# Kernel optimization log

Measured on AMD Instinct MI355X. Metric: run time of the kernel, lower is better.

Reference implementation:

```python
import jax, jax.numpy as jnp
import numpy as np

N_SYM = 128
BATCH = 131072
LEVERAGE = 30.0


def setup_inputs() -> dict:
    key = jax.random.key(0)
    ks = jax.random.split(key, 8)
    fractions = jax.random.normal(ks[0], (N_SYM, BATCH), dtype=jnp.float32)
    # exec_samples are Bernoulli(0/1) execution indicators, kept as float
    exec_samples = jnp.round(jax.random.uniform(ks[1], (N_SYM, BATCH), dtype=jnp.float32))
    pos_sizes = jax.random.normal(ks[2], (N_SYM, BATCH), dtype=jnp.float32)
    # margin rates strictly positive
    margin_rates = jax.random.uniform(ks[3], (N_SYM, BATCH), dtype=jnp.float32) * 0.9 + 0.1
    unused_margin = jax.random.uniform(ks[4], (BATCH,), dtype=jnp.float32) * 1000.0
    # per-symbol volume constraints: min == step (typical broker config), max >> min
    msm_step = jax.random.uniform(ks[5], (N_SYM,), dtype=jnp.float32) * 0.01 + 0.01
    msm_min = msm_step
    msm_max = msm_step * 1000.0
    return {
        "fractions": fractions,
        "exec_samples": exec_samples,
        "pos_sizes": pos_sizes,
        "margin_rates": margin_rates,
        "unused_margin": unused_margin,
        "msm_min": msm_min,
        "msm_step": msm_step,
        "msm_max": msm_max,
    }


def reference(fractions, exec_samples, pos_sizes, margin_rates, unused_margin,
              msm_min, msm_step, msm_max):
    """JAX port of LowLevelInferenceEngine._compute_new_pos_sizes.

    Sequential recurrence over traded symbols (axis 0), carrying
    unused_margin [BATCH]. Returns (new_pos_sizes [N_SYM, BATCH],
    final unused_margin [BATCH]).
    """

    def step_fn(um, xs):
        frac, ex, pos, mr, mn, st, mx = xs
        unused_size = um * mr * LEVERAGE
        max_pos_size = jnp.abs(pos) + unused_size
        # torch.where(pos*frac > 0, unused_size, max_pos_size).minimum(0)
        adj = jnp.minimum(jnp.where(pos * frac > 0, unused_size, max_pos_size), 0.0)
        new_pos_size = frac * (max_pos_size - adj)
        abs_nps = jnp.abs(new_pos_size)
        sgn = jnp.sign(new_pos_size)
        abs_nps = jnp.floor(abs_nps / st) * st
        abs_nps = jnp.where(abs_nps < mn, 0.0, abs_nps)
        abs_nps = jnp.minimum(abs_nps, mx)
        out = ex * (sgn * abs_nps) + (1.0 - ex) * pos
        um_new = (max_pos_size - abs_nps) / (mr * LEVERAGE)
        return um_new, out

    um_final, new_pos_sizes = jax.lax.scan(
        step_fn,
        unused_margin,
        (fractions, exec_samples, pos_sizes, margin_rates, msm_min, msm_step, msm_max),
    )
    return new_pos_sizes, um_final
```

## Files before the change

kernel.cpp:

```cpp
#include <hip/hip_runtime.h>
#include <math.h>

#define N_SYM 128
#define BATCH 131072
#define B4    (BATCH / 4)
#define LEV   30.0f
#define D     4

typedef float v4 __attribute__((ext_vector_type(4)));

__device__ __forceinline__ float step1(float f, float e, float p, float m,
                                       float st, float mn, float mx,
                                       float* um)
{
    const float mrl = m * LEV;
    const float us  = *um * mrl;
    const float mps = fabsf(p) + us;
    const float adj = fminf((p * f > 0.0f) ? us : mps, 0.0f);
    const float nps = f * (mps - adj);

    float       a  = fabsf(nps);
    const float sg = copysignf(1.0f, nps);
    a = floorf(a / st) * st;
    a = (a < mn) ? 0.0f : a;
    a = fminf(a, mx);

    *um = (mps - a) / mrl;
    return e * (sg * a) + (1.0f - e) * p;
}

__global__ __launch_bounds__(64) void lle_scan_kernel(
    const float* __restrict__ frac,
    const float* __restrict__ exs,
    const float* __restrict__ pos,
    const float* __restrict__ mrate,
    const float* __restrict__ um0,
    const float* __restrict__ msm_min,
    const float* __restrict__ msm_step,
    const float* __restrict__ msm_max,
    float* __restrict__ out)
{
    const size_t c4 = (size_t)(blockIdx.x * 64 + threadIdx.x);

    const v4* F = (const v4*)frac;
    const v4* E = (const v4*)exs;
    const v4* P = (const v4*)pos;
    const v4* M = (const v4*)mrate;
    v4*       O = (v4*)out;

    const v4 umv = __builtin_nontemporal_load((const v4*)um0 + c4);
    float um[4] = {umv.x, umv.y, umv.z, umv.w};

    v4 fb[D], eb[D], pb[D], mb[D];

#pragma unroll
    for (int j = 0; j < D; ++j) {
        const size_t o = (size_t)j * B4 + c4;
        fb[j] = __builtin_nontemporal_load(F + o);
        eb[j] = __builtin_nontemporal_load(E + o);
        pb[j] = __builtin_nontemporal_load(P + o);
        mb[j] = __builtin_nontemporal_load(M + o);
    }

    for (int s0 = 0; s0 < N_SYM - D; s0 += D) {
#pragma unroll
        for (int j = 0; j < D; ++j) {
            const int s = s0 + j;
            const v4 f = fb[j];
            const v4 e = eb[j];
            const v4 p = pb[j];
            const v4 m = mb[j];

            {
                const size_t o = (size_t)(s + D) * B4 + c4;
                fb[j] = __builtin_nontemporal_load(F + o);
                eb[j] = __builtin_nontemporal_load(E + o);
                pb[j] = __builtin_nontemporal_load(P + o);
                mb[j] = __builtin_nontemporal_load(M + o);
            }

            const float st = msm_step[s];
            const float mn = msm_min[s];
            const float mx = msm_max[s];

            v4 r;
            r.x = step1(f.x, e.x, p.x, m.x, st, mn, mx, &um[0]);
            r.y = step1(f.y, e.y, p.y, m.y, st, mn, mx, &um[1]);
            r.z = step1(f.z, e.z, p.z, m.z, st, mn, mx, &um[2]);
            r.w = step1(f.w, e.w, p.w, m.w, st, mn, mx, &um[3]);

            __builtin_nontemporal_store(r, O + (size_t)s * B4 + c4);
        }
    }

#pragma unroll
    for (int j = 0; j < D; ++j) {
        const int s = N_SYM - D + j;
        const v4 f = fb[j];
        const v4 e = eb[j];
        const v4 p = pb[j];
        const v4 m = mb[j];

        const float st = msm_step[s];
        const float mn = msm_min[s];
        const float mx = msm_max[s];

        v4 r;
        r.x = step1(f.x, e.x, p.x, m.x, st, mn, mx, &um[0]);
        r.y = step1(f.y, e.y, p.y, m.y, st, mn, mx, &um[1]);
        r.z = step1(f.z, e.z, p.z, m.z, st, mn, mx, &um[2]);
        r.w = step1(f.w, e.w, p.w, m.w, st, mn, mx, &um[3]);

        __builtin_nontemporal_store(r, O + (size_t)s * B4 + c4);
    }

    v4 umo;
    umo.x = um[0]; umo.y = um[1]; umo.z = um[2]; umo.w = um[3];
    __builtin_nontemporal_store(umo, O + (size_t)N_SYM * B4 + c4);
}

extern "C" void kernel_launch(void* const* d_in, const int* in_sizes, int n_in,
                              void* d_out, int out_size, void* d_ws, size_t ws_size,
                              hipStream_t stream) {
    const float* frac     = (const float*)d_in[0];
    const float* exs      = (const float*)d_in[1];
    const float* pos      = (const float*)d_in[2];
    const float* mrate    = (const float*)d_in[3];
    const float* um0      = (const float*)d_in[4];
    const float* msm_min  = (const float*)d_in[5];
    const float* msm_step = (const float*)d_in[6];
    const float* msm_max  = (const float*)d_in[7];
    float* out = (float*)d_out;

    const int block = 64;
    const int grid  = (BATCH / 4) / block;

    hipLaunchKernelGGL(lle_scan_kernel, dim3(grid), dim3(block), 0, stream,
                       frac, exs, pos, mrate, um0, msm_min, msm_step, msm_max,
                       out);
}
```

Measured before the change: 259.2 us.

## Add helper prefetch wavefronts that warm cache ahead of compute wave

Each block now has one compute wavefront running the scan and four helper wavefronts, one per input stream. The helpers load rows a few symbols ahead of the compute wave's progress, which they track through a shared volatile counter, so the data is already in cache when the compute wave reads it. The compute wave's loads also change from nontemporal to normal so they can hit those cached lines. The aim is to hide memory latency on the serial recurrence, at the cost of extra load traffic, spin-wait sleeps and possible cache thrashing if helpers run too far ahead.

```diff
diff --git a/kernel.cpp b/kernel.cpp
--- a/kernel.cpp
+++ b/kernel.cpp
@@ -6,6 +6,7 @@
 #define B4    (BATCH / 4)
 #define LEV   30.0f
 #define D     4
+#define PD    8
 
 typedef float v4 __attribute__((ext_vector_type(4)));
 
@@ -29,7 +30,7 @@
     return e * (sg * a) + (1.0f - e) * p;
 }
 
-__global__ __launch_bounds__(64) void lle_scan_kernel(
+__global__ __launch_bounds__(320) void lle_pf_kernel(
     const float* __restrict__ frac,
     const float* __restrict__ exs,
     const float* __restrict__ pos,
@@ -40,7 +41,11 @@
     const float* __restrict__ msm_max,
     float* __restrict__ out)
 {
-    const size_t c4 = (size_t)(blockIdx.x * 64 + threadIdx.x);
+    __shared__ volatile int prog;
+
+    const int    wv   = threadIdx.x >> 6;
+    const int    lane = threadIdx.x & 63;
+    const size_t c4   = (size_t)blockIdx.x * 64 + lane;
 
     const v4* F = (const v4*)frac;
     const v4* E = (const v4*)exs;
@@ -48,36 +53,57 @@
     const v4* M = (const v4*)mrate;
     v4*       O = (v4*)out;
 
-    const v4 umv = __builtin_nontemporal_load((const v4*)um0 + c4);
-    float um[4] = {umv.x, umv.y, umv.z, umv.w};
+    if (wv == 0) {
+        if (lane == 0) prog = -1;
 
-    v4 fb[D], eb[D], pb[D], mb[D];
+        const v4 umv = *((const v4*)um0 + c4);
+        float um[4] = {umv.x, umv.y, umv.z, umv.w};
+
+        v4 fb[D], eb[D], pb[D], mb[D];
 
 #pragma unroll
-    for (int j = 0; j < D; ++j) {
-        const size_t o = (size_t)j * B4 + c4;
-        fb[j] = __builtin_nontemporal_load(F + o);
-        eb[j] = __builtin_nontemporal_load(E + o);
-        pb[j] = __builtin_nontemporal_load(P + o);
-        mb[j] = __builtin_nontemporal_load(M + o);
-    }
+        for (int j = 0; j < D; ++j) {
+            const size_t o = (size_t)j * B4 + c4;
+            fb[j] = F[o]; eb[j] = E[o]; pb[j] = P[o]; mb[j] = M[o];
+        }
 
-    for (int s0 = 0; s0 < N_SYM - D; s0 += D) {
+        for (int s0 = 0; s0 < N_SYM - D; s0 += D) {
+#pragma unroll
+            for (int j = 0; j < D; ++j) {
+                const int s = s0 + j;
+                if (lane == 0) prog = s;
+                const v4 f = fb[j];
+                const v4 e = eb[j];
+                const v4 p = pb[j];
+                const v4 m = mb[j];
+
+                {
+                    const size_t o = (size_t)(s + D) * B4 + c4;
+                    fb[j] = F[o]; eb[j] = E[o]; pb[j] = P[o]; mb[j] = M[o];
+                }
+
+                const float st = msm_step[s];
+                const float mn = msm_min[s];
+                const float mx = msm_max[s];
+
+                v4 r;
+                r.x = step1(f.x, e.x, p.x, m.x, st, mn, mx, &um[0]);
+                r.y = step1(f.y, e.y, p.y, m.y, st, mn, mx, &um[1]);
+                r.z = step1(f.z, e.z, p.z, m.z, st, mn, mx, &um[2]);
+                r.w = step1(f.w, e.w, p.w, m.w, st, mn, mx, &um[3]);
+
+                __builtin_nontemporal_store(r, O + (size_t)s * B4 + c4);
+            }
+        }
+
 #pragma unroll
         for (int j = 0; j < D; ++j) {
-            const int s = s0 + j;
+            const int s = N_SYM - D + j;
+            if (lane == 0) prog = s;
             const v4 f = fb[j];
             const v4 e = eb[j];
             const v4 p = pb[j];
             const v4 m = mb[j];
-
-            {
-                const size_t o = (size_t)(s + D) * B4 + c4;
-                fb[j] = __builtin_nontemporal_load(F + o);
-                eb[j] = __builtin_nontemporal_load(E + o);
-                pb[j] = __builtin_nontemporal_load(P + o);
-                mb[j] = __builtin_nontemporal_load(M + o);
-            }
 
             const float st = msm_step[s];
             const float mn = msm_min[s];
@@ -91,32 +117,26 @@
 
             __builtin_nontemporal_store(r, O + (size_t)s * B4 + c4);
         }
+
+        v4 umo;
+        umo.x = um[0]; umo.y = um[1]; umo.z = um[2]; umo.w = um[3];
+        __builtin_nontemporal_store(umo, O + (size_t)N_SYM * B4 + c4);
+    } else {
+        const v4* SRC = (wv == 1) ? F : (wv == 2) ? E : (wv == 3) ? P : M;
+
+        __builtin_amdgcn_s_sleep(32);
+
+        for (int g = 0; g < N_SYM / 4; ++g) {
+            const int s = g * 4;
+            while (s > prog + PD) __builtin_amdgcn_s_sleep(8);
+
+            const v4 a = SRC[(size_t)(s + 0) * B4 + c4];
+            const v4 b = SRC[(size_t)(s + 1) * B4 + c4];
+            const v4 c = SRC[(size_t)(s + 2) * B4 + c4];
+            const v4 d = SRC[(size_t)(s + 3) * B4 + c4];
+            asm volatile("" :: "v"(a), "v"(b), "v"(c), "v"(d));
+        }
     }
-
-#pragma unroll
-    for (int j = 0; j < D; ++j) {
-        const int s = N_SYM - D + j;
-        const v4 f = fb[j];
-        const v4 e = eb[j];
-        const v4 p = pb[j];
-        const v4 m = mb[j];
-
-        const float st = msm_step[s];
-        const float mn = msm_min[s];
-        const float mx = msm_max[s];
-
-        v4 r;
-        r.x = step1(f.x, e.x, p.x, m.x, st, mn, mx, &um[0]);
-        r.y = step1(f.y, e.y, p.y, m.y, st, mn, mx, &um[1]);
-        r.z = step1(f.z, e.z, p.z, m.z, st, mn, mx, &um[2]);
-        r.w = step1(f.w, e.w, p.w, m.w, st, mn, mx, &um[3]);
-
-        __builtin_nontemporal_store(r, O + (size_t)s * B4 + c4);
-    }
-
-    v4 umo;
-    umo.x = um[0]; umo.y = um[1]; umo.z = um[2]; umo.w = um[3];
-    __builtin_nontemporal_store(umo, O + (size_t)N_SYM * B4 + c4);
 }
 
 extern "C" void kernel_launch(void* const* d_in, const int* in_sizes, int n_in,
@@ -132,10 +152,10 @@
     const float* msm_max  = (const float*)d_in[7];
     float* out = (float*)d_out;
 
-    const int block = 64;
-    const int grid  = (BATCH / 4) / block;
+    const int block = 320;
+    const int grid  = (BATCH / 4) / 64;
 
-    hipLaunchKernelGGL(lle_scan_kernel, dim3(grid), dim3(block), 0, stream,
+    hipLaunchKernelGGL(lle_pf_kernel, dim3(grid), dim3(block), 0, stream,
                        frac, exs, pos, mrate, um0, msm_min, msm_step, msm_max,
                        out);
 }
```

New measurement: 285.0 us. +9.9%, slower.
